# Performance work log

Hardware: AMD Instinct MI355X
Metric: run time of the kernel (lower is better)

## Reference

```python
import jax, jax.numpy as jnp
import numpy as np

RATE = 0.5

def setup_inputs() -> dict:
    key = jax.random.key(0)
    k1, k2, k3 = jax.random.split(key, 3)
    B, N, F = 4, 4096, 256
    Xs = jax.random.normal(k1, (B, N, F), dtype=jnp.float32)
    As = jax.random.uniform(k2, (B, N, N), dtype=jnp.float32)
    w = jax.random.normal(k3, (F, 1), dtype=jnp.float32)
    return {"Xs": Xs, "As": As, "w": w}

def reference(Xs, As, w):
    B, N, F = Xs.shape
    keep = max(int(RATE * N), 1)
    # graph-conv score: (A @ X) @ w -> [B, N, 1]
    support = jnp.einsum('bnm,bmf->bnf', As, Xs)
    logits = jnp.einsum('bnf,fo->bno', support, w)[..., 0]   # [B, N]
    # softmax over node axis (axis=1 of [B,N,1] == node axis); single head -> mean is identity
    scoring = jax.nn.softmax(logits, axis=1)                 # [B, N]
    keep_values, keep_idx = jax.lax.top_k(scoring, keep)     # [B, K]
    # dual gather: pooled node features and adjacency submatrix
    Xs_out = jnp.take_along_axis(Xs, keep_idx[:, :, None], axis=1)        # [B, K, F]
    A_rows = jnp.take_along_axis(As, keep_idx[:, :, None], axis=1)        # [B, K, N]
    As_out = jnp.take_along_axis(A_rows, keep_idx[:, None, :], axis=2)    # [B, K, K]
    return Xs_out, As_out, keep_values
```

## Files before the change

### kernel.cpp

```cpp
#include <hip/hip_runtime.h>
#include <math.h>

#define N_NODES 4096
#define F_DIM 256
#define KEEP 2048
#define B_SZ 4

__device__ inline unsigned f64_to_f32_bits_rne(double x) {
    if (!(x > 0.0)) return 0u;
    if (x >= 0x1p-126) {
        unsigned long long xb = __double_as_longlong(x);
        int E = (int)((xb >> 52) & 0x7FFull) - 1023;
        unsigned long long mant = xb & 0xFFFFFFFFFFFFFull;
        unsigned m23 = (unsigned)(mant >> 29);
        unsigned long long rem = mant & ((1ull << 29) - 1ull);
        const unsigned long long half = 1ull << 28;
        if (rem > half || (rem == half && (m23 & 1u))) {
            m23++;
            if (m23 == (1u << 23)) { m23 = 0u; E++; }
        }
        return ((unsigned)(E + 127) << 23) | m23;
    } else {
        double r = x * 0x1p149;
        double ri = rint(r);
        return (unsigned)ri;
    }
}

__device__ inline double f32_bits_to_f64(unsigned b) {
    int e = (int)((b >> 23) & 0xFFu);
    unsigned m = b & 0x7FFFFFu;
    if (e == 0) return (double)m * 0x1p-149;
    return ldexp((double)(m | 0x800000u), e - 150);
}

__global__ __launch_bounds__(256) void k_xw(const float* __restrict__ Xs,
                                            const float* __restrict__ w,
                                            double* __restrict__ xw) {
    int wave = threadIdx.x >> 6;
    int lane = threadIdx.x & 63;
    int row  = blockIdx.x * 4 + wave;
    const float4* xr = (const float4*)(Xs + (size_t)row * F_DIM);
    const float4* wr = (const float4*)w;
    float4 x  = xr[lane];
    float4 ww = wr[lane];
    double s = (double)x.x*ww.x + (double)x.y*ww.y + (double)x.z*ww.z + (double)x.w*ww.w;
    #pragma unroll
    for (int off = 32; off > 0; off >>= 1) s += __shfl_xor(s, off, 64);
    if (lane == 0) xw[row] = s;
}

__global__ __launch_bounds__(256) void k_logits(const float* __restrict__ A,
                                                const double* __restrict__ xw,
                                                double* __restrict__ logits) {
    int row = blockIdx.x;
    int b   = row >> 12;
    const float4*  ar = (const float4*)(A + (size_t)row * N_NODES);
    const double*  xr = xw + b * N_NODES;
    int t = threadIdx.x;
    double s = 0.0;
    #pragma unroll
    for (int it = 0; it < 4; ++it) {
        int i4 = it * 256 + t;
        float4 a = ar[i4];
        const double* xp = xr + i4 * 4;
        s += a.x*xp[0] + a.y*xp[1] + a.z*xp[2] + a.w*xp[3];
    }
    #pragma unroll
    for (int off = 32; off > 0; off >>= 1) s += __shfl_xor(s, off, 64);
    __shared__ double red[4];
    if ((t & 63) == 0) red[t >> 6] = s;
    __syncthreads();
    if (t == 0) logits[row] = red[0] + red[1] + red[2] + red[3];
}

__global__ __launch_bounds__(1024) void k_topk(const double* __restrict__ logits,
                                               int* __restrict__ keep_idx,
                                               unsigned* __restrict__ keep_val_bits) {
    int b = blockIdx.x;
    int t = threadIdx.x;
    int wave = t >> 6, lane = t & 63;
    __shared__ unsigned qb[N_NODES];
    __shared__ int nz[N_NODES];
    __shared__ double wredd[16];
    __shared__ int wredi[16];
    const double* L = logits + b * N_NODES;

    float lmax = -INFINITY;
    #pragma unroll
    for (int k = 0; k < 4; ++k) {
        int i = t + k * 1024;
        float v = (float)L[i];
        qb[i] = __float_as_uint(v);
        lmax = fmaxf(lmax, v);
    }
    #pragma unroll
    for (int off = 32; off > 0; off >>= 1) lmax = fmaxf(lmax, __shfl_xor(lmax, off, 64));
    if (lane == 0) wredd[wave] = (double)lmax;
    __syncthreads();
    float m = (float)wredd[0];
    #pragma unroll
    for (int i = 1; i < 16; ++i) m = fmaxf(m, (float)wredd[i]);
    __syncthreads();

    double lsum = 0.0;
    #pragma unroll
    for (int k = 0; k < 4; ++k) {
        int i = t + k * 1024;
        float d = __uint_as_float(qb[i]) - m;
        unsigned ebits = 0u;
        if (d >= -87.3365402f) {
            ebits = f64_to_f32_bits_rne(exp((double)d));
            if (ebits < 0x00800000u) ebits = 0u;
        }
        qb[i] = ebits;
        lsum += f32_bits_to_f64(ebits);
    }
    #pragma unroll
    for (int off = 32; off > 0; off >>= 1) lsum += __shfl_xor(lsum, off, 64);
    if (lane == 0) wredd[wave] = lsum;
    __syncthreads();
    double S64 = 0.0;
    #pragma unroll
    for (int i = 0; i < 16; ++i) S64 += wredd[i];
    double Sv = f32_bits_to_f64(f64_to_f32_bits_rne(S64));

    #pragma unroll
    for (int k = 0; k < 4; ++k) {
        int i = t + k * 1024;
        qb[i] = f64_to_f32_bits_rne(f32_bits_to_f64(qb[i]) / Sv);
    }
    __syncthreads();

    int i0 = 4 * t;
    unsigned s0 = qb[i0], s1 = qb[i0+1], s2 = qb[i0+2], s3 = qb[i0+3];
    int f0 = (s0 == 0u), f1 = (s1 == 0u), f2 = (s2 == 0u), f3 = (s3 == 0u);
    int mysum = f0 + f1 + f2 + f3;
    int inc = mysum;
    #pragma unroll
    for (int off = 1; off < 64; off <<= 1) {
        int u = __shfl_up(inc, off, 64);
        if (lane >= off) inc += u;
    }
    if (lane == 63) wredi[wave] = inc;
    __syncthreads();
    int waveoff = 0, Z = 0;
    for (int j = 0; j < 16; ++j) { int v = wredi[j]; Z += v; if (j < wave) waveoff += v; }
    int C = N_NODES - Z;
    int ez = waveoff + inc - mysum;

    unsigned sv4[4] = {s0, s1, s2, s3};
    int fl4[4] = {f0, f1, f2, f3};
    #pragma unroll
    for (int k = 0; k < 4; ++k) {
        int i = i0 + k;
        if (fl4[k]) {
            int r = C + ez;
            if (r < KEEP) { keep_idx[b*KEEP + r] = i; keep_val_bits[b*KEEP + r] = 0u; }
            ez++;
        } else {
            nz[i - ez] = i;
        }
    }
    __syncthreads();

    for (int p = t; p < C; p += 1024) {
        int i = nz[p];
        unsigned sv = qb[i];
        int rank = 0;
        for (int p2 = 0; p2 < C; ++p2) {
            int j = nz[p2];
            unsigned sj = qb[j];
            rank += (sj > sv) || (sj == sv && j < i);
        }
        if (rank < KEEP) { keep_idx[b*KEEP + rank] = i; keep_val_bits[b*KEEP + rank] = sv; }
    }
}

__global__ __launch_bounds__(256) void k_gatherX(const float* __restrict__ Xs,
                                                 const int* __restrict__ keep_idx,
                                                 float* __restrict__ Xout) {
    int wave = threadIdx.x >> 6;
    int lane = threadIdx.x & 63;
    int r = blockIdx.x * 4 + wave;
    int b = r >> 11;
    int src = keep_idx[r];
    const float4* in  = (const float4*)(Xs + ((size_t)(b * N_NODES + src)) * F_DIM);
    float4*       out = (float4*)(Xout + (size_t)r * F_DIM);
    out[lane] = in[lane];
}

__global__ __launch_bounds__(256) void k_gatherA(const float* __restrict__ A,
                                                 const int* __restrict__ keep_idx,
                                                 float* __restrict__ Aout) {
    int r = blockIdx.x;
    int b = r >> 11;
    int src = keep_idx[r];
    __shared__ float row[N_NODES];
    const float4* in = (const float4*)(A + ((size_t)(b * N_NODES + src)) * N_NODES);
    float4* rowv = (float4*)row;
    int t = threadIdx.x;
    #pragma unroll
    for (int it = 0; it < 4; ++it) rowv[it * 256 + t] = in[it * 256 + t];
    __syncthreads();
    const int* idx = keep_idx + b * KEEP;
    float* out = Aout + (size_t)r * KEEP;
    #pragma unroll
    for (int q = 0; q < 8; ++q) {
        int j = q * 256 + t;
        out[j] = row[idx[j]];
    }
}

extern "C" void kernel_launch(void* const* d_in, const int* in_sizes, int n_in,
                              void* d_out, int out_size, void* d_ws, size_t ws_size,
                              hipStream_t stream) {
    const float* Xs = (const float*)d_in[0];
    const float* As = (const float*)d_in[1];
    const float* w  = (const float*)d_in[2];

    float* out  = (float*)d_out;
    float* Xout = out;
    float* Aout = out + (size_t)B_SZ * KEEP * F_DIM;
    unsigned* KV = (unsigned*)(Aout + (size_t)B_SZ * KEEP * KEEP);

    char* ws = (char*)d_ws;
    double* xw       = (double*)ws;
    double* logits   = (double*)(ws + 131072);
    int*    keep_idx = (int*)(ws + 262144);

    k_xw     <<<B_SZ * N_NODES / 4, 256, 0, stream>>>(Xs, w, xw);
    k_logits <<<B_SZ * N_NODES,     256, 0, stream>>>(As, xw, logits);
    k_topk   <<<B_SZ,              1024, 0, stream>>>(logits, keep_idx, KV);
    k_gatherX<<<B_SZ * KEEP / 4,    256, 0, stream>>>(Xs, keep_idx, Xout);
    k_gatherA<<<B_SZ * KEEP,        256, 0, stream>>>(As, keep_idx, Aout);
}
```

Baseline: 107.6 us.

## Process four rows per block in logits and merge the two gather kernels

The logits kernel now has each block compute four adjacent rows of A against the shared xw vector, so each xw double is loaded once per four rows instead of once per row. The block count drops by four. The X and A gather kernels are merged into one launch that branches on block index, which removes one kernel launch. Since xw is small and cached, the main gain is expected from fewer launches and less per-row reduction overhead, and it costs more registers per thread.

```diff
diff --git a/kernel.cpp b/kernel.cpp
--- a/kernel.cpp
+++ b/kernel.cpp
@@ -5,6 +5,7 @@
 #define F_DIM 256
 #define KEEP 2048
 #define B_SZ 4
+#define LROWS 4
 
 __device__ inline unsigned f64_to_f32_bits_rne(double x) {
     if (!(x > 0.0)) return 0u;
@@ -53,25 +54,41 @@
 __global__ __launch_bounds__(256) void k_logits(const float* __restrict__ A,
                                                 const double* __restrict__ xw,
                                                 double* __restrict__ logits) {
-    int row = blockIdx.x;
-    int b   = row >> 12;
-    const float4*  ar = (const float4*)(A + (size_t)row * N_NODES);
+    int rb = blockIdx.x * LROWS;
+    int b  = rb >> 12;
+    int t  = threadIdx.x;
+    const float4*  ar = (const float4*)(A + (size_t)rb * N_NODES);
     const double*  xr = xw + b * N_NODES;
-    int t = threadIdx.x;
-    double s = 0.0;
+    double s0 = 0.0, s1 = 0.0, s2 = 0.0, s3 = 0.0;
     #pragma unroll
     for (int it = 0; it < 4; ++it) {
         int i4 = it * 256 + t;
-        float4 a = ar[i4];
         const double* xp = xr + i4 * 4;
-        s += a.x*xp[0] + a.y*xp[1] + a.z*xp[2] + a.w*xp[3];
-    }
-    #pragma unroll
-    for (int off = 32; off > 0; off >>= 1) s += __shfl_xor(s, off, 64);
-    __shared__ double red[4];
-    if ((t & 63) == 0) red[t >> 6] = s;
-    __syncthreads();
-    if (t == 0) logits[row] = red[0] + red[1] + red[2] + red[3];
+        double x0 = xp[0], x1 = xp[1], x2 = xp[2], x3 = xp[3];
+        float4 a0 = ar[i4];
+        float4 a1 = ar[1024 + i4];
+        float4 a2 = ar[2048 + i4];
+        float4 a3 = ar[3072 + i4];
+        s0 += a0.x*x0 + a0.y*x1 + a0.z*x2 + a0.w*x3;
+        s1 += a1.x*x0 + a1.y*x1 + a1.z*x2 + a1.w*x3;
+        s2 += a2.x*x0 + a2.y*x1 + a2.z*x2 + a2.w*x3;
+        s3 += a3.x*x0 + a3.y*x1 + a3.z*x2 + a3.w*x3;
+    }
+    #pragma unroll
+    for (int off = 32; off > 0; off >>= 1) {
+        s0 += __shfl_xor(s0, off, 64);
+        s1 += __shfl_xor(s1, off, 64);
+        s2 += __shfl_xor(s2, off, 64);
+        s3 += __shfl_xor(s3, off, 64);
+    }
+    __shared__ double red[LROWS][4];
+    int wave = t >> 6;
+    if ((t & 63) == 0) {
+        red[0][wave] = s0; red[1][wave] = s1; red[2][wave] = s2; red[3][wave] = s3;
+    }
+    __syncthreads();
+    if (t < LROWS)
+        logits[rb + t] = red[t][0] + red[t][1] + red[t][2] + red[t][3];
 }
 
 __global__ __launch_bounds__(1024) void k_topk(const double* __restrict__ logits,
@@ -149,7 +166,6 @@
     int C = N_NODES - Z;
     int ez = waveoff + inc - mysum;
 
-    unsigned sv4[4] = {s0, s1, s2, s3};
     int fl4[4] = {f0, f1, f2, f3};
     #pragma unroll
     for (int k = 0; k < 4; ++k) {
@@ -177,38 +193,38 @@
     }
 }
 
-__global__ __launch_bounds__(256) void k_gatherX(const float* __restrict__ Xs,
-                                                 const int* __restrict__ keep_idx,
-                                                 float* __restrict__ Xout) {
-    int wave = threadIdx.x >> 6;
-    int lane = threadIdx.x & 63;
-    int r = blockIdx.x * 4 + wave;
-    int b = r >> 11;
-    int src = keep_idx[r];
-    const float4* in  = (const float4*)(Xs + ((size_t)(b * N_NODES + src)) * F_DIM);
-    float4*       out = (float4*)(Xout + (size_t)r * F_DIM);
-    out[lane] = in[lane];
-}
-
-__global__ __launch_bounds__(256) void k_gatherA(const float* __restrict__ A,
-                                                 const int* __restrict__ keep_idx,
-                                                 float* __restrict__ Aout) {
-    int r = blockIdx.x;
-    int b = r >> 11;
-    int src = keep_idx[r];
+#define XBLKS (B_SZ * KEEP / 4)
+__global__ __launch_bounds__(256) void k_gather(const float* __restrict__ Xs,
+                                                const float* __restrict__ As,
+                                                const int* __restrict__ keep_idx,
+                                                float* __restrict__ Xout,
+                                                float* __restrict__ Aout) {
     __shared__ float row[N_NODES];
-    const float4* in = (const float4*)(A + ((size_t)(b * N_NODES + src)) * N_NODES);
-    float4* rowv = (float4*)row;
     int t = threadIdx.x;
-    #pragma unroll
-    for (int it = 0; it < 4; ++it) rowv[it * 256 + t] = in[it * 256 + t];
-    __syncthreads();
-    const int* idx = keep_idx + b * KEEP;
-    float* out = Aout + (size_t)r * KEEP;
-    #pragma unroll
-    for (int q = 0; q < 8; ++q) {
-        int j = q * 256 + t;
-        out[j] = row[idx[j]];
+    if (blockIdx.x < XBLKS) {
+        int wave = t >> 6, lane = t & 63;
+        int r = blockIdx.x * 4 + wave;
+        int b = r >> 11;
+        int src = keep_idx[r];
+        const float4* in  = (const float4*)(Xs + ((size_t)(b * N_NODES + src)) * F_DIM);
+        float4*       out = (float4*)(Xout + (size_t)r * F_DIM);
+        out[lane] = in[lane];
+    } else {
+        int r = blockIdx.x - XBLKS;
+        int b = r >> 11;
+        int src = keep_idx[r];
+        const float4* in = (const float4*)(As + ((size_t)(b * N_NODES + src)) * N_NODES);
+        float4* rowv = (float4*)row;
+        #pragma unroll
+        for (int it = 0; it < 4; ++it) rowv[it * 256 + t] = in[it * 256 + t];
+        __syncthreads();
+        const int* idx = keep_idx + b * KEEP;
+        float* outp = Aout + (size_t)r * KEEP;
+        #pragma unroll
+        for (int q = 0; q < 8; ++q) {
+            int j = q * 256 + t;
+            outp[j] = row[idx[j]];
+        }
     }
 }
 
@@ -229,9 +245,8 @@
     double* logits   = (double*)(ws + 131072);
     int*    keep_idx = (int*)(ws + 262144);
 
-    k_xw     <<<B_SZ * N_NODES / 4, 256, 0, stream>>>(Xs, w, xw);
-    k_logits <<<B_SZ * N_NODES,     256, 0, stream>>>(As, xw, logits);
-    k_topk   <<<B_SZ,              1024, 0, stream>>>(logits, keep_idx, KV);
-    k_gatherX<<<B_SZ * KEEP / 4,    256, 0, stream>>>(Xs, keep_idx, Xout);
-    k_gatherA<<<B_SZ * KEEP,        256, 0, stream>>>(As, keep_idx, Aout);
-}
+    k_xw     <<<B_SZ * N_NODES / 4,      256, 0, stream>>>(Xs, w, xw);
+    k_logits <<<B_SZ * N_NODES / LROWS,  256, 0, stream>>>(As, xw, logits);
+    k_topk   <<<B_SZ,                   1024, 0, stream>>>(logits, keep_idx, KV);
+    k_gather <<<XBLKS + B_SZ * KEEP,     256, 0, stream>>>(Xs, As, keep_idx, Xout, Aout);
+}
```

Result: faster. 90.34 us (-16.0%).
